# Optimization experiments

Hardware: AMD Instinct MI355X
Metric: run time of the kernel (lower is better)

The kernel has to match this reference:

```python
import jax, jax.numpy as jnp
import numpy as np

N_NODES = 50000
N_EDGES = 400000
IN_DIM = 256
EPS_BN = 1e-5


def _bn(x, gamma, beta):
    # BatchNorm over nodes (training-mode batch statistics)
    m = jnp.mean(x, axis=0)
    v = jnp.var(x, axis=0)
    return (x - m) * jax.lax.rsqrt(v + EPS_BN) * gamma + beta


def _gcn(x, W, b, src, dst, n):
    # PyG GCNConv: add self-loops, symmetric deg^-1/2 normalization
    h = x @ W  # [N, F_out]
    deg = jax.ops.segment_sum(jnp.ones_like(dst, dtype=h.dtype), dst, num_segments=n) + 1.0
    dinv = jax.lax.rsqrt(deg)
    coef = dinv[src] * dinv[dst]  # [E]
    agg = jax.ops.segment_sum(h[src] * coef[:, None], dst, num_segments=n)
    agg = agg + h * (dinv * dinv)[:, None]  # self-loop contribution
    return agg + b


def _gat(x, W, a_src, a_dst, b, src, dst, n):
    # PyG GATConv, heads=H, concat=False (mean over heads)
    H, F = a_src.shape
    h = (x @ W).reshape(n, H, F)
    asc = jnp.einsum('nhf,hf->nh', h, a_src)
    adc = jnp.einsum('nhf,hf->nh', h, a_dst)
    loops = jnp.arange(n, dtype=src.dtype)
    s = jnp.concatenate([src, loops])
    d = jnp.concatenate([dst, loops])
    e = jax.nn.leaky_relu(asc[s] + adc[d], 0.2)  # [E+N, H]
    mx = jax.ops.segment_max(e, d, num_segments=n)
    ee = jnp.exp(e - mx[d])
    denom = jax.ops.segment_sum(ee, d, num_segments=n)
    alpha = ee / (denom[d] + 1e-16)  # edge softmax over incoming edges
    out = jax.ops.segment_sum(alpha[:, :, None] * h[s], d, num_segments=n)  # [N,H,F]
    return out.mean(axis=1) + b


def setup_inputs() -> dict:
    key = jax.random.key(0)
    ks = jax.random.split(key, 24)

    def glorot(k, shape):
        fan = shape[0] + shape[-1]
        return jax.random.normal(k, shape, jnp.float32) * np.sqrt(2.0 / fan)

    d = {}
    d['x'] = jax.random.normal(ks[0], (N_NODES, IN_DIM), jnp.float32)
    d['edge_index'] = jax.random.randint(ks[1], (2, N_EDGES), 0, N_NODES, jnp.int32)
    # GCNConv 1: 256 -> 256
    d['w1'] = glorot(ks[2], (IN_DIM, 256)); d['b1'] = jnp.zeros((256,), jnp.float32)
    d['g1'] = jnp.ones((256,), jnp.float32); d['be1'] = jnp.zeros((256,), jnp.float32)
    # GATConv: 256 -> 128, heads=4, concat=False
    d['gat_w'] = glorot(ks[3], (256, 4 * 128))
    d['gat_as'] = glorot(ks[4], (4, 128))
    d['gat_ad'] = glorot(ks[5], (4, 128))
    d['gat_b'] = jnp.zeros((128,), jnp.float32)
    d['g2'] = jnp.ones((128,), jnp.float32); d['be2'] = jnp.zeros((128,), jnp.float32)
    # GCNConv 3..5
    d['w3'] = glorot(ks[6], (128, 64)); d['b3'] = jnp.zeros((64,), jnp.float32)
    d['g3'] = jnp.ones((64,), jnp.float32); d['be3'] = jnp.zeros((64,), jnp.float32)
    d['w4'] = glorot(ks[7], (64, 32)); d['b4'] = jnp.zeros((32,), jnp.float32)
    d['g4'] = jnp.ones((32,), jnp.float32); d['be4'] = jnp.zeros((32,), jnp.float32)
    d['w5'] = glorot(ks[8], (32, 16)); d['b5'] = jnp.zeros((16,), jnp.float32)
    d['g5'] = jnp.ones((16,), jnp.float32); d['be5'] = jnp.zeros((16,), jnp.float32)
    # FC head
    d['fw1'] = glorot(ks[9], (16, 8)); d['fb1'] = jnp.zeros((8,), jnp.float32)
    d['fw2'] = glorot(ks[10], (8, 3)); d['fb2'] = jnp.zeros((3,), jnp.float32)
    return d


def reference(x, edge_index, w1, b1, g1, be1, gat_w, gat_as, gat_ad, gat_b, g2, be2,
              w3, b3, g3, be3, w4, b4, g4, be4, w5, b5, g5, be5, fw1, fb1, fw2, fb2):
    n = x.shape[0]
    src, dst = edge_index[0], edge_index[1]
    lrelu = lambda h: jax.nn.leaky_relu(h, 0.01)
    # dropout is identity in eval mode
    h = lrelu(_bn(_gcn(x, w1, b1, src, dst, n), g1, be1))
    h = lrelu(_bn(_gat(h, gat_w, gat_as, gat_ad, gat_b, src, dst, n), g2, be2))
    h = lrelu(_bn(_gcn(h, w3, b3, src, dst, n), g3, be3))
    h = lrelu(_bn(_gcn(h, w4, b4, src, dst, n), g4, be4))
    h = lrelu(_bn(_gcn(h, w5, b5, src, dst, n), g5, be5))
    h = lrelu(h @ fw1 + fb1)
    h = h @ fw2 + fb2
    return jax.nn.log_softmax(h, axis=1)
```

## Files before the change

### kernel.cpp

```cpp
#include <hip/hip_runtime.h>

#define NN 50000
#define NE 400000
#define GSTAT 2048

typedef short bf16x8 __attribute__((ext_vector_type(8)));
typedef float f32x4 __attribute__((ext_vector_type(4)));

__device__ __forceinline__ float lrelu01(float v) { return v >= 0.f ? v : 0.01f * v; }
__device__ __forceinline__ float lrelu02(float v) { return v >= 0.f ? v : 0.2f * v; }

__device__ __forceinline__ ushort f2bf(float f) {
  union { float f; unsigned u; } v; v.f = f;
  unsigned u = v.u;
  return (ushort)((u + 0x7FFFu + ((u >> 16) & 1u)) >> 16);
}
__device__ __forceinline__ float bf2f(ushort u) {
  union { unsigned u; float f; } v; v.u = ((unsigned)u) << 16;
  return v.f;
}

__global__ void wprep(const float* __restrict__ w1, const float* __restrict__ gw,
                      const float* __restrict__ w3, const float* __restrict__ w4,
                      const float* __restrict__ w5,
                      ushort* __restrict__ w1T, ushort* __restrict__ gwT,
                      ushort* __restrict__ w3T, ushort* __restrict__ w4T,
                      ushort* __restrict__ w5T) {
  int i = blockIdx.x * 256 + threadIdx.x;
  const float* W; ushort* WT; int K, N, j;
  if (i < 65536)        { W = w1; WT = w1T; K = 256; N = 256; j = i; }
  else if (i < 196608)  { W = gw; WT = gwT; K = 256; N = 512; j = i - 65536; }
  else if (i < 204800)  { W = w3; WT = w3T; K = 128; N = 64;  j = i - 196608; }
  else if (i < 206848)  { W = w4; WT = w4T; K = 64;  N = 32;  j = i - 204800; }
  else if (i < 207360)  { W = w5; WT = w5T; K = 32;  N = 16;  j = i - 206848; }
  else return;
  int k = j / N, c = j % N;
  WT[(size_t)c * K + k] = f2bf(W[(size_t)j]);
}

__global__ void count_kernel(const int* __restrict__ dst, int* __restrict__ counts, int e) {
  int i = blockIdx.x * 256 + threadIdx.x;
  if (i < e) atomicAdd(&counts[dst[i]], 1);
}

__global__ __launch_bounds__(256) void block_count_sum(const int* __restrict__ counts,
                                                       int* __restrict__ bsum,
                                                       float* __restrict__ dinv, int n) {
  int i = blockIdx.x * 256 + threadIdx.x;
  int c = (i < n) ? counts[i] : 0;
  if (i < n) dinv[i] = rsqrtf((float)c + 1.0f);
  int s = c;
#pragma unroll
  for (int off = 32; off > 0; off >>= 1) s += __shfl_down(s, off);
  __shared__ int ws[4];
  if ((threadIdx.x & 63) == 0) ws[threadIdx.x >> 6] = s;
  __syncthreads();
  if (threadIdx.x == 0) bsum[blockIdx.x] = ws[0] + ws[1] + ws[2] + ws[3];
}

__global__ __launch_bounds__(256) void scan_bsum(int* __restrict__ bsum, int nb) {
  __shared__ int sh[256];
  int v = (threadIdx.x < nb) ? bsum[threadIdx.x] : 0;
  sh[threadIdx.x] = v;
  __syncthreads();
  for (int off = 1; off < 256; off <<= 1) {
    int t = (threadIdx.x >= off) ? sh[threadIdx.x - off] : 0;
    __syncthreads();
    sh[threadIdx.x] += t;
    __syncthreads();
  }
  if (threadIdx.x < nb) bsum[threadIdx.x] = sh[threadIdx.x] - v;
}

__global__ __launch_bounds__(256) void row_start_kernel(const int* __restrict__ counts,
                                                        const int* __restrict__ bsum,
                                                        int* __restrict__ row_start, int n) {
  __shared__ int sh[256];
  int i = blockIdx.x * 256 + threadIdx.x;
  int c = (i < n) ? counts[i] : 0;
  sh[threadIdx.x] = c;
  __syncthreads();
  for (int off = 1; off < 256; off <<= 1) {
    int t = (threadIdx.x >= off) ? sh[threadIdx.x - off] : 0;
    __syncthreads();
    sh[threadIdx.x] += t;
    __syncthreads();
  }
  int incl = sh[threadIdx.x];
  int base = bsum[blockIdx.x];
  if (i < n) row_start[i] = base + incl - c;
  if (i == n - 1) row_start[n] = base + incl;
}

__global__ void fill_kernel(const int* __restrict__ src, const int* __restrict__ dst,
                            const int* __restrict__ row_start, int* __restrict__ cursor,
                            int* __restrict__ csr, int e) {
  int i = blockIdx.x * 256 + threadIdx.x;
  if (i >= e) return;
  int d = dst[i];
  int pos = atomicAdd(&cursor[d], 1);
  csr[row_start[d] + pos] = src[i];
}

__global__ __launch_bounds__(256) void gemm_mfma_x(const float* __restrict__ A,
                                                   const ushort* __restrict__ BT,
                                                   ushort* __restrict__ C,
                                                   int M, int K, int N,
                                                   const float* __restrict__ rowscale) {
  __shared__ ushort As[128][40];
  __shared__ ushort Bs[128][40];
  const int tid = threadIdx.x;
  const int bm = blockIdx.x * 128;
  const int bn = blockIdx.y * 128;
  const int wave = tid >> 6, lane = tid & 63;
  const int wr = (wave >> 1) * 64;
  const int wc = (wave & 1) * 64;
  const int lr = lane & 15;
  const int lk = (lane >> 4) * 8;

  f32x4 acc[4][4];
#pragma unroll
  for (int m = 0; m < 4; ++m)
#pragma unroll
    for (int n = 0; n < 4; ++n)
#pragma unroll
      for (int q = 0; q < 4; ++q) acc[m][n][q] = 0.f;

  for (int k0 = 0; k0 < K; k0 += 32) {
#pragma unroll
    for (int it = 0; it < 2; ++it) {
      int s = tid + it * 256;
      int r = s >> 2;
      int c = (s & 3) * 8;
      int grow = bm + r; if (grow >= M) grow = M - 1;
      float4 va = *reinterpret_cast<const float4*>(&A[(size_t)grow * K + k0 + c]);
      float4 vb = *reinterpret_cast<const float4*>(&A[(size_t)grow * K + k0 + c + 4]);
      ushort4 lo = make_ushort4(f2bf(va.x), f2bf(va.y), f2bf(va.z), f2bf(va.w));
      ushort4 hi = make_ushort4(f2bf(vb.x), f2bf(vb.y), f2bf(vb.z), f2bf(vb.w));
      *reinterpret_cast<ushort4*>(&As[r][c]) = lo;
      *reinterpret_cast<ushort4*>(&As[r][c + 4]) = hi;
    }
#pragma unroll
    for (int it = 0; it < 2; ++it) {
      int s = tid + it * 256;
      int r = s >> 2;
      int c = (s & 3) * 8;
      int4 v = *reinterpret_cast<const int4*>(&BT[(size_t)(bn + r) * K + k0 + c]);
      *reinterpret_cast<int4*>(&Bs[r][c]) = v;
    }
    __syncthreads();

    bf16x8 af[4], bfr[4];
#pragma unroll
    for (int m = 0; m < 4; ++m)
      af[m] = *reinterpret_cast<const bf16x8*>(&As[wr + m * 16 + lr][lk]);
#pragma unroll
    for (int n = 0; n < 4; ++n)
      bfr[n] = *reinterpret_cast<const bf16x8*>(&Bs[wc + n * 16 + lr][lk]);
#pragma unroll
    for (int m = 0; m < 4; ++m)
#pragma unroll
      for (int n = 0; n < 4; ++n)
        acc[m][n] = __builtin_amdgcn_mfma_f32_16x16x32_bf16(af[m], bfr[n], acc[m][n], 0, 0, 0);
    __syncthreads();
  }

  const int rbase = (lane >> 4) * 4;
  const int cbase = lane & 15;
#pragma unroll
  for (int m = 0; m < 4; ++m) {
#pragma unroll
    for (int q = 0; q < 4; ++q) {
      int row = bm + wr + m * 16 + rbase + q;
      if (row >= M) continue;
      float sc = rowscale ? rowscale[row] : 1.f;
#pragma unroll
      for (int n = 0; n < 4; ++n) {
        int col = bn + wc + n * 16 + cbase;
        C[(size_t)row * N + col] = f2bf(acc[m][n][q] * sc);
      }
    }
  }
}

__global__ __launch_bounds__(256) void gemm_mfma_bn(const ushort* __restrict__ A,
                                                    const ushort* __restrict__ BT,
                                                    ushort* __restrict__ C,
                                                    int M, int K, int N,
                                                    const float* __restrict__ rowscale,
                                                    const float* __restrict__ stats,
                                                    const float* __restrict__ gamma,
                                                    const float* __restrict__ beta) {
  __shared__ ushort As[128][40];
  __shared__ ushort Bs[128][40];
  __shared__ float scl[256], shl[256];
  const int tid = threadIdx.x;
  const float inv_n = 1.0f / (float)NN;
  for (int k = tid; k < K; k += 256) {
    float mean = stats[k] * inv_n;
    float var = stats[K + k] * inv_n - mean * mean;
    float sc = gamma[k] * rsqrtf(var + 1e-5f);
    scl[k] = sc;
    shl[k] = beta[k] - mean * sc;
  }
  const int bm = blockIdx.x * 128;
  const int bn = blockIdx.y * 128;
  const int wave = tid >> 6, lane = tid & 63;
  const int wr = (wave >> 1) * 64;
  const int wc = (wave & 1) * 64;
  const int lr = lane & 15;
  const int lk = (lane >> 4) * 8;

  f32x4 acc[4][4];
#pragma unroll
  for (int m = 0; m < 4; ++m)
#pragma unroll
    for (int n = 0; n < 4; ++n)
#pragma unroll
      for (int q = 0; q < 4; ++q) acc[m][n][q] = 0.f;
  __syncthreads();

  for (int k0 = 0; k0 < K; k0 += 32) {
#pragma unroll
    for (int it = 0; it < 2; ++it) {
      int s = tid + it * 256;
      int r = s >> 2;
      int c = (s & 3) * 8;
      int grow = bm + r; if (grow >= M) grow = M - 1;
      int4 v = *reinterpret_cast<const int4*>(&A[(size_t)grow * K + k0 + c]);
      ushort* u = reinterpret_cast<ushort*>(&v);
      ushort tmp[8];
#pragma unroll
      for (int j = 0; j < 8; ++j) {
        float f = bf2f(u[j]) * scl[k0 + c + j] + shl[k0 + c + j];
        tmp[j] = f2bf(f >= 0.f ? f : 0.01f * f);
      }
      *reinterpret_cast<int4*>(&As[r][c]) = *reinterpret_cast<int4*>(tmp);
    }
#pragma unroll
    for (int it = 0; it < 2; ++it) {
      int s = tid + it * 256;
      int r = s >> 2;
      int c = (s & 3) * 8;
      int4 v = *reinterpret_cast<const int4*>(&BT[(size_t)(bn + r) * K + k0 + c]);
      *reinterpret_cast<int4*>(&Bs[r][c]) = v;
    }
    __syncthreads();

    bf16x8 af[4], bfr[4];
#pragma unroll
    for (int m = 0; m < 4; ++m)
      af[m] = *reinterpret_cast<const bf16x8*>(&As[wr + m * 16 + lr][lk]);
#pragma unroll
    for (int n = 0; n < 4; ++n)
      bfr[n] = *reinterpret_cast<const bf16x8*>(&Bs[wc + n * 16 + lr][lk]);
#pragma unroll
    for (int m = 0; m < 4; ++m)
#pragma unroll
      for (int n = 0; n < 4; ++n)
        acc[m][n] = __builtin_amdgcn_mfma_f32_16x16x32_bf16(af[m], bfr[n], acc[m][n], 0, 0, 0);
    __syncthreads();
  }

  const int rbase = (lane >> 4) * 4;
  const int cbase = lane & 15;
#pragma unroll
  for (int m = 0; m < 4; ++m) {
#pragma unroll
    for (int q = 0; q < 4; ++q) {
      int row = bm + wr + m * 16 + rbase + q;
      if (row >= M) continue;
      float sc = rowscale ? rowscale[row] : 1.f;
#pragma unroll
      for (int n = 0; n < 4; ++n) {
        int col = bn + wc + n * 16 + cbase;
        C[(size_t)row * N + col] = f2bf(acc[m][n][q] * sc);
      }
    }
  }
}

template <int TN>
__global__ __launch_bounds__(256) void gemm_mfma_n_bn(const ushort* __restrict__ A,
                                                      const ushort* __restrict__ BT,
                                                      ushort* __restrict__ C,
                                                      int M, int K,
                                                      const float* __restrict__ rowscale,
                                                      const float* __restrict__ stats,
                                                      const float* __restrict__ gamma,
                                                      const float* __restrict__ beta) {
  __shared__ ushort As[128][40];
  __shared__ ushort Bs[TN][40];
  __shared__ float scl[128], shl[128];
  const int tid = threadIdx.x;
  const float inv_n = 1.0f / (float)NN;
  if (tid < K) {
    float mean = stats[tid] * inv_n;
    float var = stats[K + tid] * inv_n - mean * mean;
    float sc = gamma[tid] * rsqrtf(var + 1e-5f);
    scl[tid] = sc;
    shl[tid] = beta[tid] - mean * sc;
  }
  const int bm = blockIdx.x * 128;
  const int wave = tid >> 6, lane = tid & 63;
  const int wr = wave * 32;
  const int lr = lane & 15;
  const int lk = (lane >> 4) * 8;
  constexpr int NF = TN / 16;

  f32x4 acc[2][NF];
#pragma unroll
  for (int m = 0; m < 2; ++m)
#pragma unroll
    for (int n = 0; n < NF; ++n)
#pragma unroll
      for (int q = 0; q < 4; ++q) acc[m][n][q] = 0.f;
  __syncthreads();

  for (int k0 = 0; k0 < K; k0 += 32) {
#pragma unroll
    for (int it = 0; it < 2; ++it) {
      int s = tid + it * 256;
      int r = s >> 2;
      int c = (s & 3) * 8;
      int grow = bm + r; if (grow >= M) grow = M - 1;
      int4 v = *reinterpret_cast<const int4*>(&A[(size_t)grow * K + k0 + c]);
      ushort* u = reinterpret_cast<ushort*>(&v);
      ushort tmp[8];
#pragma unroll
      for (int j = 0; j < 8; ++j) {
        float f = bf2f(u[j]) * scl[k0 + c + j] + shl[k0 + c + j];
        tmp[j] = f2bf(f >= 0.f ? f : 0.01f * f);
      }
      *reinterpret_cast<int4*>(&As[r][c]) = *reinterpret_cast<int4*>(tmp);
    }
    if (tid < TN * 4) {
      int r = tid >> 2;
      int c = (tid & 3) * 8;
      int4 v = *reinterpret_cast<const int4*>(&BT[(size_t)r * K + k0 + c]);
      *reinterpret_cast<int4*>(&Bs[r][c]) = v;
    }
    __syncthreads();

    bf16x8 af[2], bfr[NF];
#pragma unroll
    for (int m = 0; m < 2; ++m)
      af[m] = *reinterpret_cast<const bf16x8*>(&As[wr + m * 16 + lr][lk]);
#pragma unroll
    for (int n = 0; n < NF; ++n)
      bfr[n] = *reinterpret_cast<const bf16x8*>(&Bs[n * 16 + lr][lk]);
#pragma unroll
    for (int m = 0; m < 2; ++m)
#pragma unroll
      for (int n = 0; n < NF; ++n)
        acc[m][n] = __builtin_amdgcn_mfma_f32_16x16x32_bf16(af[m], bfr[n], acc[m][n], 0, 0, 0);
    __syncthreads();
  }

  const int rbase = (lane >> 4) * 4;
  const int cbase = lane & 15;
#pragma unroll
  for (int m = 0; m < 2; ++m) {
#pragma unroll
    for (int q = 0; q < 4; ++q) {
      int row = bm + wr + m * 16 + rbase + q;
      if (row >= M) continue;
      float sc = rowscale ? rowscale[row] : 1.f;
#pragma unroll
      for (int n = 0; n < NF; ++n) {
        int col = n * 16 + cbase;
        C[(size_t)row * TN + col] = f2bf(acc[m][n][q] * sc);
      }
    }
  }
}

template <int F>
__global__ __launch_bounds__(256) void gcn_agg_stats(const ushort* __restrict__ h,
                                                     const int* __restrict__ row_start,
                                                     const int* __restrict__ csr,
                                                     const float* __restrict__ dinv,
                                                     ushort* __restrict__ out,
                                                     float* __restrict__ partials, int n) {
  constexpr int TPN = F / 4;
  constexpr int NPB = 256 / TPN;
  const int tid = threadIdx.x;
  const int sub = tid / TPN;
  const int f4 = (tid % TPN) * 4;
  float ps0 = 0.f, ps1 = 0.f, ps2 = 0.f, ps3 = 0.f;
  float pq0 = 0.f, pq1 = 0.f, pq2 = 0.f, pq3 = 0.f;

  for (int node = blockIdx.x * NPB + sub; node < n; node += GSTAT * NPB) {
    float di = dinv[node];
    ushort4 sv = *reinterpret_cast<const ushort4*>(&h[(size_t)node * F + f4]);
    float a0 = bf2f(sv.x), a1 = bf2f(sv.y), a2 = bf2f(sv.z), a3 = bf2f(sv.w);
    int s0 = row_start[node], s1 = row_start[node + 1];
    int e = s0;
    for (; e + 1 < s1; e += 2) {
      int sA = csr[e], sB = csr[e + 1];
      ushort4 vA = *reinterpret_cast<const ushort4*>(&h[(size_t)sA * F + f4]);
      ushort4 vB = *reinterpret_cast<const ushort4*>(&h[(size_t)sB * F + f4]);
      a0 += bf2f(vA.x) + bf2f(vB.x);
      a1 += bf2f(vA.y) + bf2f(vB.y);
      a2 += bf2f(vA.z) + bf2f(vB.z);
      a3 += bf2f(vA.w) + bf2f(vB.w);
    }
    if (e < s1) {
      int sA = csr[e];
      ushort4 vA = *reinterpret_cast<const ushort4*>(&h[(size_t)sA * F + f4]);
      a0 += bf2f(vA.x); a1 += bf2f(vA.y); a2 += bf2f(vA.z); a3 += bf2f(vA.w);
    }
    a0 *= di; a1 *= di; a2 *= di; a3 *= di;
    ushort4 o = make_ushort4(f2bf(a0), f2bf(a1), f2bf(a2), f2bf(a3));
    *reinterpret_cast<ushort4*>(&out[(size_t)node * F + f4]) = o;
    ps0 += a0; ps1 += a1; ps2 += a2; ps3 += a3;
    pq0 += a0 * a0; pq1 += a1 * a1; pq2 += a2 * a2; pq3 += a3 * a3;
  }

  __shared__ float red[8][256];
  red[0][tid] = ps0; red[1][tid] = ps1; red[2][tid] = ps2; red[3][tid] = ps3;
  red[4][tid] = pq0; red[5][tid] = pq1; red[6][tid] = pq2; red[7][tid] = pq3;
  __syncthreads();
#pragma unroll
  for (int half = 128; half >= TPN; half >>= 1) {
    if (tid < half) {
#pragma unroll
      for (int k = 0; k < 8; ++k) red[k][tid] += red[k][tid + half];
    }
    __syncthreads();
  }
  if (tid < TPN) {
    int b = blockIdx.x;
#pragma unroll
    for (int j = 0; j < 4; ++j) {
      partials[(size_t)(tid * 4 + j) * GSTAT + b] = red[j][tid];
      partials[(size_t)(F + tid * 4 + j) * GSTAT + b] = red[4 + j][tid];
    }
  }
}

__global__ __launch_bounds__(256) void gat_agg_stats(const ushort* __restrict__ hg,
                                                     const int* __restrict__ row_start,
                                                     const int* __restrict__ csr,
                                                     const float* __restrict__ alpha,
                                                     const float* __restrict__ wself,
                                                     const float* __restrict__ invden,
                                                     ushort* __restrict__ out,
                                                     float* __restrict__ partials, int n) {
  const int tid = threadIdx.x;
  const int wave = tid >> 6;
  const int lane = tid & 63;
  const int f2 = lane * 2;
  float ps0 = 0.f, ps1 = 0.f, pq0 = 0.f, pq1 = 0.f;

  for (int node = blockIdx.x * 4 + wave; node < n; node += GSTAT * 4) {
    float4 idv = *reinterpret_cast<const float4*>(&invden[node * 4]);
    float4 wsv = *reinterpret_cast<const float4*>(&wself[node * 4]);
    float a0, a1;
    {
      const ushort* hrow = hg + (size_t)node * 512;
      ushort2 v0 = *reinterpret_cast<const ushort2*>(&hrow[f2]);
      ushort2 v1 = *reinterpret_cast<const ushort2*>(&hrow[128 + f2]);
      ushort2 v2 = *reinterpret_cast<const ushort2*>(&hrow[256 + f2]);
      ushort2 v3 = *reinterpret_cast<const ushort2*>(&hrow[384 + f2]);
      float c0 = wsv.x * idv.x, c1 = wsv.y * idv.y, c2 = wsv.z * idv.z, c3 = wsv.w * idv.w;
      a0 = c0 * bf2f(v0.x) + c1 * bf2f(v1.x) + c2 * bf2f(v2.x) + c3 * bf2f(v3.x);
      a1 = c0 * bf2f(v0.y) + c1 * bf2f(v1.y) + c2 * bf2f(v2.y) + c3 * bf2f(v3.y);
    }
    int s0 = row_start[node], s1 = row_start[node + 1];
    int e = s0;
    for (; e + 1 < s1; e += 2) {
      int sA = csr[e], sB = csr[e + 1];
      float4 alA = *reinterpret_cast<const float4*>(&alpha[(size_t)e * 4]);
      float4 alB = *reinterpret_cast<const float4*>(&alpha[(size_t)(e + 1) * 4]);
      const ushort* rA = hg + (size_t)sA * 512;
      const ushort* rB = hg + (size_t)sB * 512;
      ushort2 A0 = *reinterpret_cast<const ushort2*>(&rA[f2]);
      ushort2 A1 = *reinterpret_cast<const ushort2*>(&rA[128 + f2]);
      ushort2 A2 = *reinterpret_cast<const ushort2*>(&rA[256 + f2]);
      ushort2 A3 = *reinterpret_cast<const ushort2*>(&rA[384 + f2]);
      ushort2 B0 = *reinterpret_cast<const ushort2*>(&rB[f2]);
      ushort2 B1 = *reinterpret_cast<const ushort2*>(&rB[128 + f2]);
      ushort2 B2 = *reinterpret_cast<const ushort2*>(&rB[256 + f2]);
      ushort2 B3 = *reinterpret_cast<const ushort2*>(&rB[384 + f2]);
      float cA0 = alA.x * idv.x, cA1 = alA.y * idv.y, cA2 = alA.z * idv.z, cA3 = alA.w * idv.w;
      float cB0 = alB.x * idv.x, cB1 = alB.y * idv.y, cB2 = alB.z * idv.z, cB3 = alB.w * idv.w;
      a0 += cA0 * bf2f(A0.x) + cA1 * bf2f(A1.x) + cA2 * bf2f(A2.x) + cA3 * bf2f(A3.x)
          + cB0 * bf2f(B0.x) + cB1 * bf2f(B1.x) + cB2 * bf2f(B2.x) + cB3 * bf2f(B3.x);
      a1 += cA0 * bf2f(A0.y) + cA1 * bf2f(A1.y) + cA2 * bf2f(A2.y) + cA3 * bf2f(A3.y)
          + cB0 * bf2f(B0.y) + cB1 * bf2f(B1.y) + cB2 * bf2f(B2.y) + cB3 * bf2f(B3.y);
    }
    if (e < s1) {
      int sA = csr[e];
      float4 alA = *reinterpret_cast<const float4*>(&alpha[(size_t)e * 4]);
      const ushort* rA = hg + (size_t)sA * 512;
      ushort2 A0 = *reinterpret_cast<const ushort2*>(&rA[f2]);
      ushort2 A1 = *reinterpret_cast<const ushort2*>(&rA[128 + f2]);
      ushort2 A2 = *reinterpret_cast<const ushort2*>(&rA[256 + f2]);
      ushort2 A3 = *reinterpret_cast<const ushort2*>(&rA[384 + f2]);
      float cA0 = alA.x * idv.x, cA1 = alA.y * idv.y, cA2 = alA.z * idv.z, cA3 = alA.w * idv.w;
      a0 += cA0 * bf2f(A0.x) + cA1 * bf2f(A1.x) + cA2 * bf2f(A2.x) + cA3 * bf2f(A3.x);
      a1 += cA0 * bf2f(A0.y) + cA1 * bf2f(A1.y) + cA2 * bf2f(A2.y) + cA3 * bf2f(A3.y);
    }
    a0 *= 0.25f; a1 *= 0.25f;
    ushort2 o = make_ushort2(f2bf(a0), f2bf(a1));
    *reinterpret_cast<ushort2*>(&out[(size_t)node * 128 + f2]) = o;
    ps0 += a0; ps1 += a1; pq0 += a0 * a0; pq1 += a1 * a1;
  }

  __shared__ float red[4][256];
  red[0][tid] = ps0; red[1][tid] = ps1; red[2][tid] = pq0; red[3][tid] = pq1;
  __syncthreads();
#pragma unroll
  for (int half = 128; half >= 64; half >>= 1) {
    if (tid < half) {
#pragma unroll
      for (int k = 0; k < 4; ++k) red[k][tid] += red[k][tid + half];
    }
    __syncthreads();
  }
  if (tid < 64) {
    int b = blockIdx.x;
    partials[(size_t)(tid * 2 + 0) * GSTAT + b] = red[0][tid];
    partials[(size_t)(tid * 2 + 1) * GSTAT + b] = red[1][tid];
    partials[(size_t)(128 + tid * 2 + 0) * GSTAT + b] = red[2][tid];
    partials[(size_t)(128 + tid * 2 + 1) * GSTAT + b] = red[3][tid];
  }
}

__global__ __launch_bounds__(256) void bn_reduce_col(const float* __restrict__ partials,
                                                     float* __restrict__ stats) {
  int c = blockIdx.x;
  float s = 0.f;
  for (int b = threadIdx.x; b < GSTAT; b += 256) s += partials[(size_t)c * GSTAT + b];
#pragma unroll
  for (int off = 32; off > 0; off >>= 1) s += __shfl_down(s, off);
  __shared__ float ws[4];
  if ((threadIdx.x & 63) == 0) ws[threadIdx.x >> 6] = s;
  __syncthreads();
  if (threadIdx.x == 0) stats[c] = ws[0] + ws[1] + ws[2] + ws[3];
}

__global__ __launch_bounds__(256) void gat_scores_bf(const ushort* __restrict__ hg,
                                                     const float* __restrict__ a_src,
                                                     const float* __restrict__ a_dst,
                                                     float* __restrict__ asc,
                                                     float* __restrict__ adc, int n) {
  int node = blockIdx.x;
  int head = threadIdx.x >> 6;
  int lane = threadIdx.x & 63;
  ushort2 v = *reinterpret_cast<const ushort2*>(&hg[(size_t)node * 512 + head * 128 + lane * 2]);
  float v0 = bf2f(v.x), v1 = bf2f(v.y);
  float s = v0 * a_src[head * 128 + lane * 2] + v1 * a_src[head * 128 + lane * 2 + 1];
  float d = v0 * a_dst[head * 128 + lane * 2] + v1 * a_dst[head * 128 + lane * 2 + 1];
#pragma unroll
  for (int off = 32; off > 0; off >>= 1) {
    s += __shfl_down(s, off);
    d += __shfl_down(d, off);
  }
  if (lane == 0) {
    asc[node * 4 + head] = s;
    adc[node * 4 + head] = d;
  }
}

__global__ __launch_bounds__(256) void gat_softmax(const int* __restrict__ row_start,
                                                   const int* __restrict__ csr,
                                                   const float* __restrict__ asc,
                                                   const float* __restrict__ adc,
                                                   float* __restrict__ alpha,
                                                   float* __restrict__ wself,
                                                   float* __restrict__ invden, int n) {
  int i = blockIdx.x * 256 + threadIdx.x;
  if (i >= 4 * n) return;
  int node = i >> 2, h = i & 3;
  int s0 = row_start[node], s1 = row_start[node + 1];
  float ad = adc[i];
  float eself = lrelu02(asc[i] + ad);
  float m = eself;
  for (int e = s0; e < s1; ++e) {
    float v = lrelu02(asc[csr[e] * 4 + h] + ad);
    alpha[(size_t)e * 4 + h] = v;
    m = fmaxf(m, v);
  }
  float ws = __expf(eself - m);
  wself[i] = ws;
  float den = ws;
  for (int e = s0; e < s1; ++e) {
    float w = __expf(alpha[(size_t)e * 4 + h] - m);
    alpha[(size_t)e * 4 + h] = w;
    den += w;
  }
  invden[i] = 1.f / (den + 1e-16f);
}

__global__ __launch_bounds__(256) void head_kernel_bn(const ushort* __restrict__ h,
                                                      const float* __restrict__ stats,
                                                      const float* __restrict__ g5,
                                                      const float* __restrict__ be5,
                                                      const float* __restrict__ fw1,
                                                      const float* __restrict__ fb1,
                                                      const float* __restrict__ fw2,
                                                      const float* __restrict__ fb2,
                                                      float* __restrict__ out, int n) {
  __shared__ float scl[16], shl[16];
  if (threadIdx.x < 16) {
    const float inv_n = 1.0f / (float)NN;
    int k = threadIdx.x;
    float mean = stats[k] * inv_n;
    float var = stats[16 + k] * inv_n - mean * mean;
    float sc = g5[k] * rsqrtf(var + 1e-5f);
    scl[k] = sc;
    shl[k] = be5[k] - mean * sc;
  }
  __syncthreads();
  int i = blockIdx.x * 256 + threadIdx.x;
  if (i >= n) return;
  int4 ra = *reinterpret_cast<const int4*>(&h[(size_t)i * 16]);
  int4 rb = *reinterpret_cast<const int4*>(&h[(size_t)i * 16 + 8]);
  ushort u[16];
  *reinterpret_cast<int4*>(&u[0]) = ra;
  *reinterpret_cast<int4*>(&u[8]) = rb;
  float xr[16];
#pragma unroll
  for (int k = 0; k < 16; ++k) {
    float v = bf2f(u[k]) * scl[k] + shl[k];
    xr[k] = v >= 0.f ? v : 0.01f * v;
  }
  float z[8];
#pragma unroll
  for (int j = 0; j < 8; ++j) z[j] = fb1[j];
#pragma unroll
  for (int k = 0; k < 16; ++k) {
    float a = xr[k];
#pragma unroll
    for (int j = 0; j < 8; ++j) z[j] += a * fw1[k * 8 + j];
  }
#pragma unroll
  for (int j = 0; j < 8; ++j) z[j] = lrelu01(z[j]);
  float l[3];
#pragma unroll
  for (int j = 0; j < 3; ++j) l[j] = fb2[j];
#pragma unroll
  for (int k = 0; k < 8; ++k) {
    float a = z[k];
#pragma unroll
    for (int j = 0; j < 3; ++j) l[j] += a * fw2[k * 3 + j];
  }
  float mx = fmaxf(l[0], fmaxf(l[1], l[2]));
  float se = __expf(l[0] - mx) + __expf(l[1] - mx) + __expf(l[2] - mx);
  float ls = __logf(se);
#pragma unroll
  for (int j = 0; j < 3; ++j) out[(size_t)i * 3 + j] = l[j] - mx - ls;
}

extern "C" void kernel_launch(void* const* d_in, const int* in_sizes, int n_in,
                              void* d_out, int out_size, void* d_ws, size_t ws_size,
                              hipStream_t stream) {
  const float* x      = (const float*)d_in[0];
  const int*   ei     = (const int*)d_in[1];
  const int*   srcI   = ei;
  const int*   dstI   = ei + NE;
  const float* w1     = (const float*)d_in[2];
  const float* g1     = (const float*)d_in[4];
  const float* be1    = (const float*)d_in[5];
  const float* gat_w  = (const float*)d_in[6];
  const float* gat_as = (const float*)d_in[7];
  const float* gat_ad = (const float*)d_in[8];
  const float* g2     = (const float*)d_in[10];
  const float* be2    = (const float*)d_in[11];
  const float* w3     = (const float*)d_in[12];
  const float* g3     = (const float*)d_in[14];
  const float* be3    = (const float*)d_in[15];
  const float* w4     = (const float*)d_in[16];
  const float* g4     = (const float*)d_in[18];
  const float* be4    = (const float*)d_in[19];
  const float* w5     = (const float*)d_in[20];
  const float* g5     = (const float*)d_in[22];
  const float* be5    = (const float*)d_in[23];
  const float* fw1    = (const float*)d_in[24];
  const float* fb1    = (const float*)d_in[25];
  const float* fw2    = (const float*)d_in[26];
  const float* fb2    = (const float*)d_in[27];
  float* out = (float*)d_out;

  char* wsp = (char*)d_ws;
  size_t off = 0;
  auto alloc = [&](size_t bytes) -> void* {
    void* p = wsp + off;
    off += (bytes + 255) & ~(size_t)255;
    return p;
  };
  ushort* hw_bf  = (ushort*)alloc((size_t)NN * 512 * 2);
  ushort* r1     = (ushort*)alloc((size_t)NN * 256 * 2);
  ushort* r2     = (ushort*)alloc((size_t)NN * 128 * 2);
  ushort* r3     = (ushort*)alloc((size_t)NN * 64 * 2);
  ushort* r4     = (ushort*)alloc((size_t)NN * 32 * 2);
  ushort* r5     = (ushort*)alloc((size_t)NN * 16 * 2);
  ushort* w1T    = (ushort*)alloc((size_t)256 * 256 * 2);
  ushort* gwT    = (ushort*)alloc((size_t)512 * 256 * 2);
  ushort* w3T    = (ushort*)alloc((size_t)64 * 128 * 2);
  ushort* w4T    = (ushort*)alloc((size_t)32 * 64 * 2);
  ushort* w5T    = (ushort*)alloc((size_t)16 * 32 * 2);
  float*  dinv   = (float*)alloc((size_t)NN * 4);
  int*    counts = (int*)alloc((size_t)NN * 4);
  int*    cursor = (int*)alloc((size_t)NN * 4);
  int*    rstart = (int*)alloc((size_t)(NN + 4) * 4);
  int*    bsum   = (int*)alloc((size_t)256 * 4);
  int*    csr    = (int*)alloc((size_t)NE * 4);
  float*  asc    = (float*)alloc((size_t)NN * 4 * 4);
  float*  adc    = (float*)alloc((size_t)NN * 4 * 4);
  float*  wself  = (float*)alloc((size_t)NN * 4 * 4);
  float*  invden = (float*)alloc((size_t)NN * 4 * 4);
  float*  alpha  = (float*)alloc((size_t)NE * 4 * 4);
  float*  stats  = (float*)alloc(2048);
  float*  partials = (float*)alloc((size_t)512 * GSTAT * 4);

  const int egrid = (NE + 255) / 256;
  const int ngrid = (NN + 255) / 256;
  const int mblocks = (NN + 127) / 128;

  hipMemsetAsync(counts, 0, (size_t)NN * 4, stream);
  hipMemsetAsync(cursor, 0, (size_t)NN * 4, stream);
  count_kernel<<<egrid, 256, 0, stream>>>(dstI, counts, NE);
  block_count_sum<<<ngrid, 256, 0, stream>>>(counts, bsum, dinv, NN);
  scan_bsum<<<1, 256, 0, stream>>>(bsum, ngrid);
  row_start_kernel<<<ngrid, 256, 0, stream>>>(counts, bsum, rstart, NN);
  fill_kernel<<<egrid, 256, 0, stream>>>(srcI, dstI, rstart, cursor, csr, NE);

  wprep<<<810, 256, 0, stream>>>(w1, gat_w, w3, w4, w5, w1T, gwT, w3T, w4T, w5T);

  gemm_mfma_x<<<dim3(mblocks, 2), 256, 0, stream>>>(x, w1T, hw_bf, NN, 256, 256, dinv);
  gcn_agg_stats<256><<<GSTAT, 256, 0, stream>>>(hw_bf, rstart, csr, dinv, r1, partials, NN);
  bn_reduce_col<<<512, 256, 0, stream>>>(partials, stats);

  gemm_mfma_bn<<<dim3(mblocks, 4), 256, 0, stream>>>(r1, gwT, hw_bf, NN, 256, 512, nullptr,
                                                     stats, g1, be1);
  gat_scores_bf<<<NN, 256, 0, stream>>>(hw_bf, gat_as, gat_ad, asc, adc, NN);
  gat_softmax<<<(4 * NN + 255) / 256, 256, 0, stream>>>(rstart, csr, asc, adc, alpha, wself, invden, NN);
  gat_agg_stats<<<GSTAT, 256, 0, stream>>>(hw_bf, rstart, csr, alpha, wself, invden, r2, partials, NN);
  bn_reduce_col<<<256, 256, 0, stream>>>(partials, stats);

  gemm_mfma_n_bn<64><<<mblocks, 256, 0, stream>>>(r2, w3T, hw_bf, NN, 128, dinv, stats, g2, be2);
  gcn_agg_stats<64><<<GSTAT, 256, 0, stream>>>(hw_bf, rstart, csr, dinv, r3, partials, NN);
  bn_reduce_col<<<128, 256, 0, stream>>>(partials, stats);

  gemm_mfma_n_bn<32><<<mblocks, 256, 0, stream>>>(r3, w4T, hw_bf, NN, 64, dinv, stats, g3, be3);
  gcn_agg_stats<32><<<GSTAT, 256, 0, stream>>>(hw_bf, rstart, csr, dinv, r4, partials, NN);
  bn_reduce_col<<<64, 256, 0, stream>>>(partials, stats);

  gemm_mfma_n_bn<16><<<mblocks, 256, 0, stream>>>(r4, w5T, hw_bf, NN, 32, dinv, stats, g4, be4);
  gcn_agg_stats<16><<<GSTAT, 256, 0, stream>>>(hw_bf, rstart, csr, dinv, r5, partials, NN);
  bn_reduce_col<<<32, 256, 0, stream>>>(partials, stats);

  head_kernel_bn<<<ngrid, 256, 0, stream>>>(r5, stats, g5, be5, fw1, fb1, fw2, fb2, out, NN);
}
```

Measured before the change: 394.7 us.

## Fuse GAT edge softmax into aggregation and widen GCN gather loads

Removes the separate per-(node,head) softmax kernel and its alpha/wself/invden buffers. The GAT aggregation now recomputes max and denominator cooperatively per wave (16 lanes per head) with shuffle reductions, then gathers with int4 loads and reduces the heads via shuffles. The GCN aggregation moves to 8-wide bf16 loads with a 4-way unrolled edge loop and a shared-memory column reduction. Attention scores are recomputed three times per edge instead of stored, and three-quarters of the lanes sit idle during the GAT output and stats phase.

```diff
diff --git a/kernel.cpp b/kernel.cpp
--- a/kernel.cpp
+++ b/kernel.cpp
@@ -382,149 +382,164 @@
                                                      const float* __restrict__ dinv,
                                                      ushort* __restrict__ out,
                                                      float* __restrict__ partials, int n) {
-  constexpr int TPN = F / 4;
-  constexpr int NPB = 256 / TPN;
+  constexpr int LPN = F / 8;
+  constexpr int NPB = 256 / LPN;
   const int tid = threadIdx.x;
-  const int sub = tid / TPN;
-  const int f4 = (tid % TPN) * 4;
-  float ps0 = 0.f, ps1 = 0.f, ps2 = 0.f, ps3 = 0.f;
-  float pq0 = 0.f, pq1 = 0.f, pq2 = 0.f, pq3 = 0.f;
+  const int sub = tid / LPN;
+  const int f8 = (tid % LPN) * 8;
+  float ps[8], pq[8];
+#pragma unroll
+  for (int j = 0; j < 8; ++j) { ps[j] = 0.f; pq[j] = 0.f; }
 
   for (int node = blockIdx.x * NPB + sub; node < n; node += GSTAT * NPB) {
     float di = dinv[node];
-    ushort4 sv = *reinterpret_cast<const ushort4*>(&h[(size_t)node * F + f4]);
-    float a0 = bf2f(sv.x), a1 = bf2f(sv.y), a2 = bf2f(sv.z), a3 = bf2f(sv.w);
+    float a[8];
+    {
+      int4 v = *reinterpret_cast<const int4*>(&h[(size_t)node * F + f8]);
+      const ushort* u = reinterpret_cast<const ushort*>(&v);
+#pragma unroll
+      for (int j = 0; j < 8; ++j) a[j] = bf2f(u[j]);
+    }
     int s0 = row_start[node], s1 = row_start[node + 1];
+    int e = s0;
+    for (; e + 3 < s1; e += 4) {
+      int sA = csr[e], sB = csr[e + 1], sC = csr[e + 2], sD = csr[e + 3];
+      int4 vA = *reinterpret_cast<const int4*>(&h[(size_t)sA * F + f8]);
+      int4 vB = *reinterpret_cast<const int4*>(&h[(size_t)sB * F + f8]);
+      int4 vC = *reinterpret_cast<const int4*>(&h[(size_t)sC * F + f8]);
+      int4 vD = *reinterpret_cast<const int4*>(&h[(size_t)sD * F + f8]);
+      const ushort* uA = reinterpret_cast<const ushort*>(&vA);
+      const ushort* uB = reinterpret_cast<const ushort*>(&vB);
+      const ushort* uC = reinterpret_cast<const ushort*>(&vC);
+      const ushort* uD = reinterpret_cast<const ushort*>(&vD);
+#pragma unroll
+      for (int j = 0; j < 8; ++j)
+        a[j] += (bf2f(uA[j]) + bf2f(uB[j])) + (bf2f(uC[j]) + bf2f(uD[j]));
+    }
+    for (; e < s1; ++e) {
+      int sA = csr[e];
+      int4 vA = *reinterpret_cast<const int4*>(&h[(size_t)sA * F + f8]);
+      const ushort* uA = reinterpret_cast<const ushort*>(&vA);
+#pragma unroll
+      for (int j = 0; j < 8; ++j) a[j] += bf2f(uA[j]);
+    }
+    ushort u[8];
+#pragma unroll
+    for (int j = 0; j < 8; ++j) {
+      a[j] *= di;
+      u[j] = f2bf(a[j]);
+      ps[j] += a[j];
+      pq[j] += a[j] * a[j];
+    }
+    *reinterpret_cast<int4*>(&out[(size_t)node * F + f8]) = *reinterpret_cast<int4*>(u);
+  }
+
+  __shared__ float red[NPB][2 * F];
+#pragma unroll
+  for (int j = 0; j < 8; ++j) {
+    red[sub][f8 + j] = ps[j];
+    red[sub][F + f8 + j] = pq[j];
+  }
+  __syncthreads();
+  for (int c = tid; c < 2 * F; c += 256) {
+    float t = 0.f;
+#pragma unroll 4
+    for (int s = 0; s < NPB; ++s) t += red[s][c];
+    partials[(size_t)c * GSTAT + blockIdx.x] = t;
+  }
+}
+
+__global__ __launch_bounds__(256) void gat_agg_fused(const ushort* __restrict__ hg,
+                                                     const int* __restrict__ row_start,
+                                                     const int* __restrict__ csr,
+                                                     const float* __restrict__ asc,
+                                                     const float* __restrict__ adc,
+                                                     ushort* __restrict__ out,
+                                                     float* __restrict__ partials, int n) {
+  const int tid = threadIdx.x;
+  const int wave = tid >> 6, lane = tid & 63;
+  const int h = lane >> 4;
+  const int l = lane & 15;
+  const int f8 = l * 8;
+  float ps[8], pq[8];
+#pragma unroll
+  for (int j = 0; j < 8; ++j) { ps[j] = 0.f; pq[j] = 0.f; }
+
+  for (int node = blockIdx.x * 4 + wave; node < n; node += GSTAT * 4) {
+    float ad = adc[node * 4 + h];
+    float es = lrelu02(asc[node * 4 + h] + ad);
+    int s0 = row_start[node], s1 = row_start[node + 1];
+    float m = es;
+    for (int e = s0 + l; e < s1; e += 16)
+      m = fmaxf(m, lrelu02(asc[csr[e] * 4 + h] + ad));
+#pragma unroll
+    for (int off = 1; off < 16; off <<= 1) m = fmaxf(m, __shfl_xor(m, off));
+    float wself = __expf(es - m);
+    float d = (l == 0) ? wself : 0.f;
+    for (int e = s0 + l; e < s1; e += 16)
+      d += __expf(lrelu02(asc[csr[e] * 4 + h] + ad) - m);
+#pragma unroll
+    for (int off = 1; off < 16; off <<= 1) d += __shfl_xor(d, off);
+    float coef = 0.25f / (d + 1e-16f);
+    const ushort* base = hg + h * 128 + f8;
+    float a[8];
+    {
+      int4 v = *reinterpret_cast<const int4*>(base + (size_t)node * 512);
+      const ushort* u = reinterpret_cast<const ushort*>(&v);
+#pragma unroll
+      for (int j = 0; j < 8; ++j) a[j] = wself * bf2f(u[j]);
+    }
     int e = s0;
     for (; e + 1 < s1; e += 2) {
       int sA = csr[e], sB = csr[e + 1];
-      ushort4 vA = *reinterpret_cast<const ushort4*>(&h[(size_t)sA * F + f4]);
-      ushort4 vB = *reinterpret_cast<const ushort4*>(&h[(size_t)sB * F + f4]);
-      a0 += bf2f(vA.x) + bf2f(vB.x);
-      a1 += bf2f(vA.y) + bf2f(vB.y);
-      a2 += bf2f(vA.z) + bf2f(vB.z);
-      a3 += bf2f(vA.w) + bf2f(vB.w);
+      float wA = __expf(lrelu02(asc[sA * 4 + h] + ad) - m);
+      float wB = __expf(lrelu02(asc[sB * 4 + h] + ad) - m);
+      int4 vA = *reinterpret_cast<const int4*>(base + (size_t)sA * 512);
+      int4 vB = *reinterpret_cast<const int4*>(base + (size_t)sB * 512);
+      const ushort* uA = reinterpret_cast<const ushort*>(&vA);
+      const ushort* uB = reinterpret_cast<const ushort*>(&vB);
+#pragma unroll
+      for (int j = 0; j < 8; ++j) a[j] += wA * bf2f(uA[j]) + wB * bf2f(uB[j]);
     }
     if (e < s1) {
       int sA = csr[e];
-      ushort4 vA = *reinterpret_cast<const ushort4*>(&h[(size_t)sA * F + f4]);
-      a0 += bf2f(vA.x); a1 += bf2f(vA.y); a2 += bf2f(vA.z); a3 += bf2f(vA.w);
-    }
-    a0 *= di; a1 *= di; a2 *= di; a3 *= di;
-    ushort4 o = make_ushort4(f2bf(a0), f2bf(a1), f2bf(a2), f2bf(a3));
-    *reinterpret_cast<ushort4*>(&out[(size_t)node * F + f4]) = o;
-    ps0 += a0; ps1 += a1; ps2 += a2; ps3 += a3;
-    pq0 += a0 * a0; pq1 += a1 * a1; pq2 += a2 * a2; pq3 += a3 * a3;
-  }
-
-  __shared__ float red[8][256];
-  red[0][tid] = ps0; red[1][tid] = ps1; red[2][tid] = ps2; red[3][tid] = ps3;
-  red[4][tid] = pq0; red[5][tid] = pq1; red[6][tid] = pq2; red[7][tid] = pq3;
-  __syncthreads();
-#pragma unroll
-  for (int half = 128; half >= TPN; half >>= 1) {
-    if (tid < half) {
-#pragma unroll
-      for (int k = 0; k < 8; ++k) red[k][tid] += red[k][tid + half];
-    }
-    __syncthreads();
-  }
-  if (tid < TPN) {
-    int b = blockIdx.x;
-#pragma unroll
-    for (int j = 0; j < 4; ++j) {
-      partials[(size_t)(tid * 4 + j) * GSTAT + b] = red[j][tid];
-      partials[(size_t)(F + tid * 4 + j) * GSTAT + b] = red[4 + j][tid];
-    }
-  }
-}
-
-__global__ __launch_bounds__(256) void gat_agg_stats(const ushort* __restrict__ hg,
-                                                     const int* __restrict__ row_start,
-                                                     const int* __restrict__ csr,
-                                                     const float* __restrict__ alpha,
-                                                     const float* __restrict__ wself,
-                                                     const float* __restrict__ invden,
-                                                     ushort* __restrict__ out,
-                                                     float* __restrict__ partials, int n) {
-  const int tid = threadIdx.x;
-  const int wave = tid >> 6;
-  const int lane = tid & 63;
-  const int f2 = lane * 2;
-  float ps0 = 0.f, ps1 = 0.f, pq0 = 0.f, pq1 = 0.f;
-
-  for (int node = blockIdx.x * 4 + wave; node < n; node += GSTAT * 4) {
-    float4 idv = *reinterpret_cast<const float4*>(&invden[node * 4]);
-    float4 wsv = *reinterpret_cast<const float4*>(&wself[node * 4]);
-    float a0, a1;
-    {
-      const ushort* hrow = hg + (size_t)node * 512;
-      ushort2 v0 = *reinterpret_cast<const ushort2*>(&hrow[f2]);
-      ushort2 v1 = *reinterpret_cast<const ushort2*>(&hrow[128 + f2]);
-      ushort2 v2 = *reinterpret_cast<const ushort2*>(&hrow[256 + f2]);
-      ushort2 v3 = *reinterpret_cast<const ushort2*>(&hrow[384 + f2]);
-      float c0 = wsv.x * idv.x, c1 = wsv.y * idv.y, c2 = wsv.z * idv.z, c3 = wsv.w * idv.w;
-      a0 = c0 * bf2f(v0.x) + c1 * bf2f(v1.x) + c2 * bf2f(v2.x) + c3 * bf2f(v3.x);
-      a1 = c0 * bf2f(v0.y) + c1 * bf2f(v1.y) + c2 * bf2f(v2.y) + c3 * bf2f(v3.y);
-    }
-    int s0 = row_start[node], s1 = row_start[node + 1];
-    int e = s0;
-    for (; e + 1 < s1; e += 2) {
-      int sA = csr[e], sB = csr[e + 1];
-      float4 alA = *reinterpret_cast<const float4*>(&alpha[(size_t)e * 4]);
-      float4 alB = *reinterpret_cast<const float4*>(&alpha[(size_t)(e + 1) * 4]);
-      const ushort* rA = hg + (size_t)sA * 512;
-      const ushort* rB = hg + (size_t)sB * 512;
-      ushort2 A0 = *reinterpret_cast<const ushort2*>(&rA[f2]);
-      ushort2 A1 = *reinterpret_cast<const ushort2*>(&rA[128 + f2]);
-      ushort2 A2 = *reinterpret_cast<const ushort2*>(&rA[256 + f2]);
-      ushort2 A3 = *reinterpret_cast<const ushort2*>(&rA[384 + f2]);
-      ushort2 B0 = *reinterpret_cast<const ushort2*>(&rB[f2]);
-      ushort2 B1 = *reinterpret_cast<const ushort2*>(&rB[128 + f2]);
-      ushort2 B2 = *reinterpret_cast<const ushort2*>(&rB[256 + f2]);
-      ushort2 B3 = *reinterpret_cast<const ushort2*>(&rB[384 + f2]);
-      float cA0 = alA.x * idv.x, cA1 = alA.y * idv.y, cA2 = alA.z * idv.z, cA3 = alA.w * idv.w;
-      float cB0 = alB.x * idv.x, cB1 = alB.y * idv.y, cB2 = alB.z * idv.z, cB3 = alB.w * idv.w;
-      a0 += cA0 * bf2f(A0.x) + cA1 * bf2f(A1.x) + cA2 * bf2f(A2.x) + cA3 * bf2f(A3.x)
-          + cB0 * bf2f(B0.x) + cB1 * bf2f(B1.x) + cB2 * bf2f(B2.x) + cB3 * bf2f(B3.x);
-      a1 += cA0 * bf2f(A0.y) + cA1 * bf2f(A1.y) + cA2 * bf2f(A2.y) + cA3 * bf2f(A3.y)
-          + cB0 * bf2f(B0.y) + cB1 * bf2f(B1.y) + cB2 * bf2f(B2.y) + cB3 * bf2f(B3.y);
-    }
-    if (e < s1) {
-      int sA = csr[e];
-      float4 alA = *reinterpret_cast<const float4*>(&alpha[(size_t)e * 4]);
-      const ushort* rA = hg + (size_t)sA * 512;
-      ushort2 A0 = *reinterpret_cast<const ushort2*>(&rA[f2]);
-      ushort2 A1 = *reinterpret_cast<const ushort2*>(&rA[128 + f2]);
-      ushort2 A2 = *reinterpret_cast<const ushort2*>(&rA[256 + f2]);
-      ushort2 A3 = *reinterpret_cast<const ushort2*>(&rA[384 + f2]);
-      float cA0 = alA.x * idv.x, cA1 = alA.y * idv.y, cA2 = alA.z * idv.z, cA3 = alA.w * idv.w;
-      a0 += cA0 * bf2f(A0.x) + cA1 * bf2f(A1.x) + cA2 * bf2f(A2.x) + cA3 * bf2f(A3.x);
-      a1 += cA0 * bf2f(A0.y) + cA1 * bf2f(A1.y) + cA2 * bf2f(A2.y) + cA3 * bf2f(A3.y);
-    }
-    a0 *= 0.25f; a1 *= 0.25f;
-    ushort2 o = make_ushort2(f2bf(a0), f2bf(a1));
-    *reinterpret_cast<ushort2*>(&out[(size_t)node * 128 + f2]) = o;
-    ps0 += a0; ps1 += a1; pq0 += a0 * a0; pq1 += a1 * a1;
+      float wA = __expf(lrelu02(asc[sA * 4 + h] + ad) - m);
+      int4 vA = *reinterpret_cast<const int4*>(base + (size_t)sA * 512);
+      const ushort* uA = reinterpret_cast<const ushort*>(&vA);
+#pragma unroll
+      for (int j = 0; j < 8; ++j) a[j] += wA * bf2f(uA[j]);
+    }
+#pragma unroll
+    for (int j = 0; j < 8; ++j) {
+      a[j] *= coef;
+      a[j] += __shfl_xor(a[j], 16);
+      a[j] += __shfl_xor(a[j], 32);
+    }
+    if (h == 0) {
+      ushort u[8];
+#pragma unroll
+      for (int j = 0; j < 8; ++j) {
+        u[j] = f2bf(a[j]);
+        ps[j] += a[j];
+        pq[j] += a[j] * a[j];
+      }
+      *reinterpret_cast<int4*>(&out[(size_t)node * 128 + f8]) = *reinterpret_cast<int4*>(u);
+    }
   }
 
   __shared__ float red[4][256];
-  red[0][tid] = ps0; red[1][tid] = ps1; red[2][tid] = pq0; red[3][tid] = pq1;
-  __syncthreads();
-#pragma unroll
-  for (int half = 128; half >= 64; half >>= 1) {
-    if (tid < half) {
-#pragma unroll
-      for (int k = 0; k < 4; ++k) red[k][tid] += red[k][tid + half];
-    }
-    __syncthreads();
-  }
-  if (tid < 64) {
-    int b = blockIdx.x;
-    partials[(size_t)(tid * 2 + 0) * GSTAT + b] = red[0][tid];
-    partials[(size_t)(tid * 2 + 1) * GSTAT + b] = red[1][tid];
-    partials[(size_t)(128 + tid * 2 + 0) * GSTAT + b] = red[2][tid];
-    partials[(size_t)(128 + tid * 2 + 1) * GSTAT + b] = red[3][tid];
+  if (h == 0) {
+#pragma unroll
+    for (int j = 0; j < 8; ++j) {
+      red[wave][f8 + j] = ps[j];
+      red[wave][128 + f8 + j] = pq[j];
+    }
+  }
+  __syncthreads();
+  if (tid < 256) {
+    int c = tid;
+    float t = red[0][c] + red[1][c] + red[2][c] + red[3][c];
+    partials[(size_t)c * GSTAT + blockIdx.x] = t;
   }
 }
 
@@ -562,36 +577,6 @@
     asc[node * 4 + head] = s;
     adc[node * 4 + head] = d;
   }
-}
-
-__global__ __launch_bounds__(256) void gat_softmax(const int* __restrict__ row_start,
-                                                   const int* __restrict__ csr,
-                                                   const float* __restrict__ asc,
-                                                   const float* __restrict__ adc,
-                                                   float* __restrict__ alpha,
-                                                   float* __restrict__ wself,
-                                                   float* __restrict__ invden, int n) {
-  int i = blockIdx.x * 256 + threadIdx.x;
-  if (i >= 4 * n) return;
-  int node = i >> 2, h = i & 3;
-  int s0 = row_start[node], s1 = row_start[node + 1];
-  float ad = adc[i];
-  float eself = lrelu02(asc[i] + ad);
-  float m = eself;
-  for (int e = s0; e < s1; ++e) {
-    float v = lrelu02(asc[csr[e] * 4 + h] + ad);
-    alpha[(size_t)e * 4 + h] = v;
-    m = fmaxf(m, v);
-  }
-  float ws = __expf(eself - m);
-  wself[i] = ws;
-  float den = ws;
-  for (int e = s0; e < s1; ++e) {
-    float w = __expf(alpha[(size_t)e * 4 + h] - m);
-    alpha[(size_t)e * 4 + h] = w;
-    den += w;
-  }
-  invden[i] = 1.f / (den + 1e-16f);
 }
 
 __global__ __launch_bounds__(256) void head_kernel_bn(const ushort* __restrict__ h,
@@ -710,9 +695,6 @@
   int*    csr    = (int*)alloc((size_t)NE * 4);
   float*  asc    = (float*)alloc((size_t)NN * 4 * 4);
   float*  adc    = (float*)alloc((size_t)NN * 4 * 4);
-  float*  wself  = (float*)alloc((size_t)NN * 4 * 4);
-  float*  invden = (float*)alloc((size_t)NN * 4 * 4);
-  float*  alpha  = (float*)alloc((size_t)NE * 4 * 4);
   float*  stats  = (float*)alloc(2048);
   float*  partials = (float*)alloc((size_t)512 * GSTAT * 4);
 
@@ -737,8 +719,7 @@
   gemm_mfma_bn<<<dim3(mblocks, 4), 256, 0, stream>>>(r1, gwT, hw_bf, NN, 256, 512, nullptr,
                                                      stats, g1, be1);
   gat_scores_bf<<<NN, 256, 0, stream>>>(hw_bf, gat_as, gat_ad, asc, adc, NN);
-  gat_softmax<<<(4 * NN + 255) / 256, 256, 0, stream>>>(rstart, csr, asc, adc, alpha, wself, invden, NN);
-  gat_agg_stats<<<GSTAT, 256, 0, stream>>>(hw_bf, rstart, csr, alpha, wself, invden, r2, partials, NN);
+  gat_agg_fused<<<GSTAT, 256, 0, stream>>>(hw_bf, rstart, csr, asc, adc, r2, partials, NN);
   bn_reduce_col<<<256, 256, 0, stream>>>(partials, stats);
 
   gemm_mfma_n_bn<64><<<mblocks, 256, 0, stream>>>(r2, w3T, hw_bf, NN, 128, dinv, stats, g2, be2);
```

Measured after the change: 388.0 us. About the same (-1.7%).
